# Kernel optimization log

Measured on AMD Instinct MI355X. Metric: run time of the kernel, lower is better.

Reference implementation:

```python
import jax, jax.numpy as jnp
import numpy as np

N_SPANS = 4096
EMB_DIM = 384
HEADS = 4
DECAY_LAMBDA = 5.0
THRESHOLD = 0.1
NEG_SLOPE = 0.2  # PyG GATConv default leaky_relu slope


def setup_inputs() -> dict:
    key = jax.random.key(0)
    k1, k2, k3, k4, k5, k6 = jax.random.split(key, 6)
    embeddings = jax.random.normal(k1, (N_SPANS, EMB_DIM), dtype=jnp.float32)
    span_positions = jnp.sort(
        jax.random.randint(k2, (N_SPANS, 2), 0, 100000), axis=1
    ).astype(jnp.int64)
    # GATConv params: lin (no bias), per-head attention vectors, output bias
    glorot = 1.0 / np.sqrt(EMB_DIM)
    W = jax.random.normal(k3, (EMB_DIM, HEADS, EMB_DIM), dtype=jnp.float32) * glorot
    att_src = jax.random.normal(k4, (HEADS, EMB_DIM), dtype=jnp.float32) * glorot
    att_dst = jax.random.normal(k5, (HEADS, EMB_DIM), dtype=jnp.float32) * glorot
    bias = jnp.zeros((EMB_DIM,), dtype=jnp.float32)
    return {
        "embeddings": embeddings,
        "span_positions": span_positions,
        "W": W,
        "att_src": att_src,
        "att_dst": att_dst,
        "bias": bias,
    }


def _adjacency_mask(embeddings):
    # A_ij = cos_sim(e_i, e_j) * exp(-|i - j| / lambda); edges where A > 0.1
    n = embeddings.shape[0]
    en = embeddings / jnp.linalg.norm(embeddings, axis=1, keepdims=True)
    cos_sim = en @ en.T  # [N, N]
    idx = jnp.arange(n, dtype=embeddings.dtype)
    decay = jnp.exp(-jnp.abs(idx[None, :] - idx[:, None]) / DECAY_LAMBDA)
    adj = cos_sim * decay
    # diagonal is 1.0 > threshold, so self-loops (required by GATConv) are present
    return adj > THRESHOLD  # symmetric mask: mask[i, j] == edge j -> i


def reference(embeddings, span_positions, W, att_src, att_dst, bias):
    mask = _adjacency_mask(embeddings)  # [N_dst, N_src]
    # GATConv(heads=4, concat=False): project, per-head additive attention
    x = jnp.einsum("nd,dhe->nhe", embeddings, W)  # [N, H, E]
    a_src = jnp.einsum("nhe,he->nh", x, att_src)  # [N, H]
    a_dst = jnp.einsum("nhe,he->nh", x, att_dst)  # [N, H]
    # logits[i, j, h] for edge j -> i
    logits = jax.nn.leaky_relu(a_dst[:, None, :] + a_src[None, :, :], NEG_SLOPE)
    logits = jnp.where(mask[:, :, None], logits, jnp.float32(-jnp.inf))
    alpha = jax.nn.softmax(logits, axis=1)  # softmax over incoming sources j
    out = jnp.einsum("ijh,jhe->ihe", alpha, x)  # [N, H, E]
    out = out.mean(axis=1) + bias  # concat=False -> mean over heads, then bias
    return out
```

## Files before the change

### kernel.cpp

```cpp
#include <hip/hip_runtime.h>
#include <hip/hip_bf16.h>
#include <math.h>

#define N_SPANS 4096
#define EMB 384
#define HEADS 4
#define HE (HEADS * EMB)
#define BAND 11
#define BW (2 * BAND + 1)

typedef short bf16x8 __attribute__((ext_vector_type(8)));
typedef float f32x4 __attribute__((ext_vector_type(4)));

__device__ __forceinline__ unsigned short f2bf(float f) {
    union { float f; unsigned u; } x; x.f = f;
    unsigned r = x.u + 0x7fffu + ((x.u >> 16) & 1u);
    return (unsigned short)(r >> 16);
}
__device__ __forceinline__ float bf2f(unsigned short u) {
    union { unsigned u; float f; } x; x.u = ((unsigned)u) << 16; return x.f;
}

__device__ __forceinline__ float wave_sum(float v) {
    #pragma unroll
    for (int off = 32; off; off >>= 1) v += __shfl_xor(v, off, 64);
    return v;
}
__device__ __forceinline__ float wave_max(float v) {
    #pragma unroll
    for (int off = 32; off; off >>= 1) v = fmaxf(v, __shfl_xor(v, off, 64));
    return v;
}

__device__ __forceinline__ void gl2lds16(const void* g, void* l) {
    __builtin_amdgcn_global_load_lds(
        (const __attribute__((address_space(1))) void*)(uintptr_t)g,
        (__attribute__((address_space(3))) void*)(unsigned)(uintptr_t)l,
        16, 0, 0);
}

__global__ __launch_bounds__(256) void prep(const float* __restrict__ E,
                                            const float* __restrict__ W,
                                            unsigned short* __restrict__ Ebf,
                                            unsigned short* __restrict__ Wt,
                                            float* __restrict__ invn,
                                            float* __restrict__ Dots,
                                            float* __restrict__ attacc) {
    __shared__ float tile[32][33];
    const int b = blockIdx.x;
    const int tid = threadIdx.x;
    if (b < 1024) {
        const int lane = tid & 63, w = tid >> 6;
        const int n = b * 4 + w;
        const float* er = E + (size_t)n * EMB;
        const int dmax = (n >= N_SPANS - BAND) ? (N_SPANS - 1 - n) : BAND;
        const float* nb[BAND];
        #pragma unroll
        for (int d = 1; d <= BAND; ++d) {
            int j = n + d; if (j > N_SPANS - 1) j = N_SPANS - 1;
            nb[d - 1] = E + (size_t)j * EMB;
        }
        float acc[12];
        #pragma unroll
        for (int d = 0; d < 12; ++d) acc[d] = 0.f;
        float ev[6];
        #pragma unroll
        for (int m = 0; m < 6; ++m) {
            const int k = m * 64 + lane;
            const float v = er[k];
            ev[m] = v;
            acc[0] += v * v;
            #pragma unroll
            for (int d = 1; d <= BAND; ++d) {
                float u = nb[d - 1][k];
                acc[d] += (d <= dmax) ? v * u : 0.f;
            }
        }
        #pragma unroll
        for (int m = 0; m < 6; ++m)
            Ebf[(size_t)n * EMB + m * 64 + lane] = f2bf(ev[m]);
        #pragma unroll
        for (int d = 0; d < 12; ++d) acc[d] = wave_sum(acc[d]);
        float dval = 0.f;
        #pragma unroll
        for (int d = 1; d <= BAND; ++d) if (lane == d) dval = acc[d];
        if (lane >= 1 && lane <= BAND) Dots[(size_t)n * 12 + lane] = dval;
        if (lane == 0) invn[n] = 1.0f / sqrtf(acc[0]);
    } else if (b < 1600) {
        const int t = b - 1024;
        const int n0 = (t % 48) * 32;
        const int k0 = (t / 48) * 32;
        const int tx = tid & 31, ty = tid >> 5;
        #pragma unroll
        for (int q = 0; q < 4; ++q)
            tile[ty + q * 8][tx] = W[(k0 + ty + q * 8) * HE + n0 + tx];
        __syncthreads();
        #pragma unroll
        for (int q = 0; q < 4; ++q)
            Wt[(n0 + ty + q * 8) * EMB + k0 + tx] = f2bf(tile[tx][ty + q * 8]);
    } else {
        const int t = b - 1600;
        ((float4*)attacc)[t * 256 + tid] = make_float4(0.f, 0.f, 0.f, 0.f);
    }
}

__global__ __launch_bounds__(256) void gemm_attn(const unsigned short* __restrict__ Ebf,
                                                 const unsigned short* __restrict__ Wt,
                                                 const float* __restrict__ attS,
                                                 const float* __restrict__ attD,
                                                 unsigned short* __restrict__ Xb,
                                                 float* __restrict__ asrc,
                                                 float* __restrict__ adst) {
    __shared__ unsigned short As[128 * 32];
    __shared__ unsigned short Bs[128 * 32];
    const int tid = threadIdx.x;
    const int lane = tid & 63;
    const int wave = tid >> 6;
    const int m0 = blockIdx.y * 128;
    const int n0 = blockIdx.x * 128;
    const int wr = (wave >> 1) * 64;
    const int wc = (wave & 1) * 64;
    const int quad = lane >> 4;
    const int l16 = lane & 15;

    const char* Ab = (const char*)Ebf + (size_t)(m0 + wave * 32 + (lane >> 2)) * 768 + (lane & 3) * 16;
    const char* Bb = (const char*)Wt  + (size_t)(n0 + wave * 32 + (lane >> 2)) * 768 + (lane & 3) * 16;
    char* AsB = (char*)As + wave * 32 * 64;
    char* BsB = (char*)Bs + wave * 32 * 64;

    f32x4 acc[4][4];
    #pragma unroll
    for (int i = 0; i < 4; ++i)
        #pragma unroll
        for (int j = 0; j < 4; ++j) acc[i][j] = 0.f;

    for (int kt = 0; kt < 12; ++kt) {
        const int kb = kt * 64;
        __syncthreads();
        gl2lds16(Ab + kb,            AsB);
        gl2lds16(Ab + kb + 16 * 768, AsB + 16 * 64);
        gl2lds16(Bb + kb,            BsB);
        gl2lds16(Bb + kb + 16 * 768, BsB + 16 * 64);
        __syncthreads();

        bf16x8 af[4], bfr[4];
        #pragma unroll
        for (int t = 0; t < 4; ++t) {
            af[t]  = *(const bf16x8*)(&As[(wr + t * 16 + l16) * 32 + quad * 8]);
            bfr[t] = *(const bf16x8*)(&Bs[(wc + t * 16 + l16) * 32 + quad * 8]);
        }
        #pragma unroll
        for (int ti = 0; ti < 4; ++ti)
            #pragma unroll
            for (int tj = 0; tj < 4; ++tj)
                acc[ti][tj] = __builtin_amdgcn_mfma_f32_16x16x32_bf16(
                    af[ti], bfr[tj], acc[ti][tj], 0, 0, 0);
    }

    const int hblk = (n0 + wc) / EMB;
    float aS[4], aD[4];
    #pragma unroll
    for (int tj = 0; tj < 4; ++tj) {
        int col = n0 + wc + tj * 16 + l16;
        aS[tj] = attS[col];
        aD[tj] = attD[col];
    }
    #pragma unroll
    for (int ti = 0; ti < 4; ++ti)
        #pragma unroll
        for (int r = 0; r < 4; ++r) {
            float ps = 0.f, pd = 0.f;
            #pragma unroll
            for (int tj = 0; tj < 4; ++tj) {
                float v = acc[ti][tj][r];
                ps += v * aS[tj];
                pd += v * aD[tj];
            }
            #pragma unroll
            for (int off = 1; off < 16; off <<= 1) {
                ps += __shfl_xor(ps, off, 64);
                pd += __shfl_xor(pd, off, 64);
            }
            if (l16 == 0) {
                int row = m0 + wr + ti * 16 + quad * 4 + r;
                atomicAdd(&asrc[row * HEADS + hblk], ps);
                atomicAdd(&adst[row * HEADS + hblk], pd);
            }
        }

    #pragma unroll
    for (int ti = 0; ti < 4; ++ti)
        #pragma unroll
        for (int tj = 0; tj < 4; ++tj) {
            int col = n0 + wc + tj * 16 + l16;
            #pragma unroll
            for (int r = 0; r < 4; ++r) {
                int row = m0 + wr + ti * 16 + quad * 4 + r;
                Xb[row * HE + col] = f2bf(acc[ti][tj][r]);
            }
        }
}

__global__ __launch_bounds__(256) void band_attn(const float* __restrict__ invn,
                                                 const float* __restrict__ Dots,
                                                 const float* __restrict__ asrc,
                                                 const float* __restrict__ adst,
                                                 const unsigned short* __restrict__ Xb,
                                                 const float* __restrict__ bias,
                                                 float* __restrict__ out) {
    __shared__ float sAl[4][BW][4];
    __shared__ int sList[4][24];
    const int tid = threadIdx.x, lane = tid & 63, w = tid >> 6;
    const int i = blockIdx.x * 4 + w;
    const int jo = lane;
    const int j = i - BAND + jo;
    const bool inb = (jo < BW) && (j >= 0) && (j < N_SPANS);
    const int jc = inb ? j : i;

    float dotv = 0.f;
    if (inb) {
        if (jo < BAND)      dotv = Dots[(size_t)j * 12 + (BAND - jo)];
        else if (jo > BAND) dotv = Dots[(size_t)i * 12 + (jo - BAND)];
    }
    bool flag;
    if (jo == BAND) {
        flag = true;
    } else {
        int dd = jo < BAND ? BAND - jo : jo - BAND;
        float a = ((dotv * invn[i]) * invn[jc]) * expf(-(float)dd * 0.2f);
        flag = inb && (a > 0.1f);
    }

    unsigned long long mbits = __ballot(flag);
    const int cnt = __popcll(mbits);
    const int rank = __popcll(mbits & ((1ull << jo) - 1ull));
    if (flag) sList[w][rank] = jo;

    const float4 ad = ((const float4*)adst)[i];
    const float4 as = inb ? ((const float4*)asrc)[jc] : make_float4(0.f, 0.f, 0.f, 0.f);
    float al[4];
    #pragma unroll
    for (int h = 0; h < 4; ++h) {
        float z = (&ad.x)[h] + (&as.x)[h];
        z = (z >= 0.f) ? z : 0.2f * z;
        float lg = flag ? z : -INFINITY;
        float mx = wave_max(lg);
        float ex = flag ? expf(lg - mx) : 0.f;
        float sm = wave_sum(ex);
        al[h] = ex / sm;
    }
    if (flag) *(float4*)&sAl[w][jo][0] = make_float4(al[0], al[1], al[2], al[3]);

    #pragma unroll
    for (int m = 0; m < 6; ++m) {
        const int e = m * 64 + lane;
        float acc = 0.f;
        for (int ii = 0; ii < cnt; ++ii) {
            const int joL = sList[w][ii];
            const int jj = i - BAND + joL;
            const float4 a4 = *(const float4*)&sAl[w][joL][0];
            const unsigned short* xr = Xb + (size_t)jj * HE + e;
            acc += a4.x * bf2f(xr[0])   + a4.y * bf2f(xr[384])
                 + a4.z * bf2f(xr[768]) + a4.w * bf2f(xr[1152]);
        }
        out[i * EMB + e] = 0.25f * acc + bias[e];
    }
}

extern "C" void kernel_launch(void* const* d_in, const int* in_sizes, int n_in,
                              void* d_out, int out_size, void* d_ws, size_t ws_size,
                              hipStream_t stream) {
    const float* E       = (const float*)d_in[0];
    const float* W       = (const float*)d_in[2];
    const float* att_src = (const float*)d_in[3];
    const float* att_dst = (const float*)d_in[4];
    const float* bias    = (const float*)d_in[5];
    float* out = (float*)d_out;

    char* ws = (char*)d_ws;
    unsigned short* Xb  = (unsigned short*)ws;
    unsigned short* Ebf = (unsigned short*)(ws + 12582912);
    unsigned short* Wt  = (unsigned short*)(ws + 15728640);
    float* invn         = (float*)(ws + 16908288);
    float* asrc         = (float*)(ws + 16924672);
    float* adst         = (float*)(ws + 16990208);
    float* Dots         = (float*)(ws + 17055744);

    prep<<<1632, 256, 0, stream>>>(E, W, Ebf, Wt, invn, Dots, asrc );
    gemm_attn<<<dim3(12, 32), 256, 0, stream>>>(Ebf, Wt, att_src, att_dst, Xb, asrc, adst);
    band_attn<<<1024, 256, 0, stream>>>(invn, Dots, asrc, adst, Xb, bias, out);
}
```

Before: 108.7 us.

## Double-buffer LDS tiles in projection GEMM with wider K steps

New measurement: 113.5 us. +4.4%, slower.

```diff
diff --git a/kernel.cpp b/kernel.cpp
--- a/kernel.cpp
+++ b/kernel.cpp
@@ -111,22 +111,30 @@
                                                  unsigned short* __restrict__ Xb,
                                                  float* __restrict__ asrc,
                                                  float* __restrict__ adst) {
-    __shared__ unsigned short As[128 * 32];
-    __shared__ unsigned short Bs[128 * 32];
+    __shared__ unsigned short As[2][8192];
+    __shared__ unsigned short Bs[2][8192];
     const int tid = threadIdx.x;
     const int lane = tid & 63;
     const int wave = tid >> 6;
+    const int quad = lane >> 4;
+    const int l16 = lane & 15;
     const int m0 = blockIdx.y * 128;
     const int n0 = blockIdx.x * 128;
     const int wr = (wave >> 1) * 64;
     const int wc = (wave & 1) * 64;
-    const int quad = lane >> 4;
-    const int l16 = lane & 15;
-
-    const char* Ab = (const char*)Ebf + (size_t)(m0 + wave * 32 + (lane >> 2)) * 768 + (lane & 3) * 16;
-    const char* Bb = (const char*)Wt  + (size_t)(n0 + wave * 32 + (lane >> 2)) * 768 + (lane & 3) * 16;
-    char* AsB = (char*)As + wave * 32 * 64;
-    char* BsB = (char*)Bs + wave * 32 * 64;
+    const int wrB = (wave >> 1) * 8192;
+    const int wcB = (wave & 1) * 8192;
+
+    const char* aSrc[4];
+    const char* bSrc[4];
+    #pragma unroll
+    for (int q = 0; q < 4; ++q) {
+        const int c = wave * 4 + q;
+        const int rg = c >> 1;
+        const int klo = (c & 1) * 4 + quad;
+        aSrc[q] = (const char*)Ebf + (size_t)(m0 + rg * 16 + l16) * 768 + klo * 16;
+        bSrc[q] = (const char*)Wt  + (size_t)(n0 + rg * 16 + l16) * 768 + klo * 16;
+    }
 
     f32x4 acc[4][4];
     #pragma unroll
@@ -134,27 +142,47 @@
         #pragma unroll
         for (int j = 0; j < 4; ++j) acc[i][j] = 0.f;
 
-    for (int kt = 0; kt < 12; ++kt) {
-        const int kb = kt * 64;
+    #pragma unroll
+    for (int q = 0; q < 4; ++q) {
+        const int c = wave * 4 + q;
+        gl2lds16(aSrc[q], (char*)As[0] + c * 1024);
+        gl2lds16(bSrc[q], (char*)Bs[0] + c * 1024);
+    }
+    __syncthreads();
+
+    int cur = 0;
+    for (int kt = 0; kt < 6; ++kt) {
+        if (kt < 5) {
+            const int kb = (kt + 1) * 128;
+            #pragma unroll
+            for (int q = 0; q < 4; ++q) {
+                const int c = wave * 4 + q;
+                gl2lds16(aSrc[q] + kb, (char*)As[cur ^ 1] + c * 1024);
+                gl2lds16(bSrc[q] + kb, (char*)Bs[cur ^ 1] + c * 1024);
+            }
+        }
+
+        const char* aR = (const char*)As[cur] + wrB + lane * 16;
+        const char* bR = (const char*)Bs[cur] + wcB + lane * 16;
+        bf16x8 af[2][4], bfr[2][4];
+        #pragma unroll
+        for (int kk = 0; kk < 2; ++kk)
+            #pragma unroll
+            for (int t = 0; t < 4; ++t) {
+                af[kk][t]  = *(const bf16x8*)(aR + t * 2048 + kk * 1024);
+                bfr[kk][t] = *(const bf16x8*)(bR + t * 2048 + kk * 1024);
+            }
+        #pragma unroll
+        for (int kk = 0; kk < 2; ++kk)
+            #pragma unroll
+            for (int ti = 0; ti < 4; ++ti)
+                #pragma unroll
+                for (int tj = 0; tj < 4; ++tj)
+                    acc[ti][tj] = __builtin_amdgcn_mfma_f32_16x16x32_bf16(
+                        af[kk][ti], bfr[kk][tj], acc[ti][tj], 0, 0, 0);
+
         __syncthreads();
-        gl2lds16(Ab + kb,            AsB);
-        gl2lds16(Ab + kb + 16 * 768, AsB + 16 * 64);
-        gl2lds16(Bb + kb,            BsB);
-        gl2lds16(Bb + kb + 16 * 768, BsB + 16 * 64);
-        __syncthreads();
-
-        bf16x8 af[4], bfr[4];
-        #pragma unroll
-        for (int t = 0; t < 4; ++t) {
-            af[t]  = *(const bf16x8*)(&As[(wr + t * 16 + l16) * 32 + quad * 8]);
-            bfr[t] = *(const bf16x8*)(&Bs[(wc + t * 16 + l16) * 32 + quad * 8]);
-        }
-        #pragma unroll
-        for (int ti = 0; ti < 4; ++ti)
-            #pragma unroll
-            for (int tj = 0; tj < 4; ++tj)
-                acc[ti][tj] = __builtin_amdgcn_mfma_f32_16x16x32_bf16(
-                    af[ti], bfr[tj], acc[ti][tj], 0, 0, 0);
+        cur ^= 1;
     }
 
     const int hblk = (n0 + wc) / EMB;
```

## Fuse prep, GEMM and band attention into one cooperative persistent kernel

Applied to the files above, without the earlier changes.

New measurement: 230.1 us. 112% more time.

```diff
diff --git a/kernel.cpp b/kernel.cpp
--- a/kernel.cpp
+++ b/kernel.cpp
@@ -1,6 +1,9 @@
 #include <hip/hip_runtime.h>
+#include <hip/hip_cooperative_groups.h>
 #include <hip/hip_bf16.h>
 #include <math.h>
+
+namespace cg = cooperative_groups;
 
 #define N_SPANS 4096
 #define EMB 384
@@ -37,6 +40,240 @@
         (const __attribute__((address_space(1))) void*)(uintptr_t)g,
         (__attribute__((address_space(3))) void*)(unsigned)(uintptr_t)l,
         16, 0, 0);
+}
+
+__global__ __launch_bounds__(256, 2) void fused(
+    const float* __restrict__ E, const float* __restrict__ W,
+    const float* __restrict__ attS, const float* __restrict__ attD,
+    const float* __restrict__ bias,
+    unsigned short* __restrict__ Ebf, unsigned short* __restrict__ Wt,
+    float* __restrict__ invn, float* __restrict__ Dots,
+    unsigned short* __restrict__ Xb, float* __restrict__ asrc,
+    float* __restrict__ adst, float* __restrict__ out)
+{
+    __shared__ union {
+        float tile[32][33];
+        struct { unsigned short As[128 * 32]; unsigned short Bs[128 * 32]; } g;
+        struct { float sAl[4][BW][4]; int sList[4][24]; } c;
+    } sh;
+
+    cg::grid_group grid = cg::this_grid();
+    const int tid = threadIdx.x, lane = tid & 63, w = tid >> 6;
+    const int b = blockIdx.x;
+
+    for (int n = b * 4 + w; n < N_SPANS; n += 1536) {
+        const float4* er4 = (const float4*)(E + (size_t)n * EMB);
+        const int dmax = (n >= N_SPANS - BAND) ? (N_SPANS - 1 - n) : BAND;
+        const float4* nb4[BAND];
+        #pragma unroll
+        for (int d = 1; d <= BAND; ++d) {
+            int j = n + d; if (j > N_SPANS - 1) j = N_SPANS - 1;
+            nb4[d - 1] = (const float4*)(E + (size_t)j * EMB);
+        }
+        float acc[12];
+        #pragma unroll
+        for (int d = 0; d < 12; ++d) acc[d] = 0.f;
+        #pragma unroll
+        for (int mq = 0; mq < 2; ++mq) {
+            const int idx = mq * 64 + lane;
+            if (idx < 96) {
+                float4 v = er4[idx];
+                acc[0] += v.x * v.x + v.y * v.y + v.z * v.z + v.w * v.w;
+                ushort4 pb;
+                pb.x = f2bf(v.x); pb.y = f2bf(v.y); pb.z = f2bf(v.z); pb.w = f2bf(v.w);
+                ((ushort4*)(Ebf + (size_t)n * EMB))[idx] = pb;
+                #pragma unroll
+                for (int d = 1; d <= BAND; ++d) {
+                    float4 u = nb4[d - 1][idx];
+                    float dd = v.x * u.x + v.y * u.y + v.z * u.z + v.w * u.w;
+                    acc[d] += (d <= dmax) ? dd : 0.f;
+                }
+            }
+        }
+        #pragma unroll
+        for (int d = 0; d < 12; ++d) acc[d] = wave_sum(acc[d]);
+        float dval = 0.f;
+        #pragma unroll
+        for (int d = 1; d <= BAND; ++d) if (lane == d) dval = acc[d];
+        if (lane >= 1 && lane <= BAND) Dots[(size_t)n * 12 + lane] = dval;
+        if (lane == 0) invn[n] = 1.0f / sqrtf(acc[0]);
+    }
+
+    {
+        const int tx = tid & 31, ty = tid >> 5;
+        for (int t = b; t < 576; t += 384) {
+            const int n0t = (t % 48) * 32, k0 = (t / 48) * 32;
+            __syncthreads();
+            #pragma unroll
+            for (int q = 0; q < 4; ++q)
+                sh.tile[ty + q * 8][tx] = W[(k0 + ty + q * 8) * HE + n0t + tx];
+            __syncthreads();
+            #pragma unroll
+            for (int q = 0; q < 4; ++q)
+                Wt[(n0t + ty + q * 8) * EMB + k0 + tx] = f2bf(sh.tile[tx][ty + q * 8]);
+        }
+    }
+
+    if (b >= 192 && b < 224)
+        ((float4*)asrc)[(b - 192) * 256 + tid] = make_float4(0.f, 0.f, 0.f, 0.f);
+
+    grid.sync();
+
+    {
+        const int m0 = (b / 12) * 128;
+        const int n0 = (b % 12) * 128;
+        const int wave = w;
+        const int quad = lane >> 4;
+        const int l16 = lane & 15;
+        const int wr = (wave >> 1) * 64;
+        const int wc = (wave & 1) * 64;
+
+        const char* Ab = (const char*)Ebf + (size_t)(m0 + wave * 32 + (lane >> 2)) * 768 + (lane & 3) * 16;
+        const char* Bb = (const char*)Wt  + (size_t)(n0 + wave * 32 + (lane >> 2)) * 768 + (lane & 3) * 16;
+        char* AsB = (char*)sh.g.As + wave * 32 * 64;
+        char* BsB = (char*)sh.g.Bs + wave * 32 * 64;
+
+        f32x4 acc[4][4];
+        #pragma unroll
+        for (int i = 0; i < 4; ++i)
+            #pragma unroll
+            for (int j = 0; j < 4; ++j) acc[i][j] = 0.f;
+
+        for (int kt = 0; kt < 12; ++kt) {
+            const int kb = kt * 64;
+            __syncthreads();
+            gl2lds16(Ab + kb,            AsB);
+            gl2lds16(Ab + kb + 16 * 768, AsB + 16 * 64);
+            gl2lds16(Bb + kb,            BsB);
+            gl2lds16(Bb + kb + 16 * 768, BsB + 16 * 64);
+            __syncthreads();
+
+            bf16x8 af[4], bfr[4];
+            #pragma unroll
+            for (int t = 0; t < 4; ++t) {
+                af[t]  = *(const bf16x8*)(&sh.g.As[(wr + t * 16 + l16) * 32 + quad * 8]);
+                bfr[t] = *(const bf16x8*)(&sh.g.Bs[(wc + t * 16 + l16) * 32 + quad * 8]);
+            }
+            #pragma unroll
+            for (int ti = 0; ti < 4; ++ti)
+                #pragma unroll
+                for (int tj = 0; tj < 4; ++tj)
+                    acc[ti][tj] = __builtin_amdgcn_mfma_f32_16x16x32_bf16(
+                        af[ti], bfr[tj], acc[ti][tj], 0, 0, 0);
+        }
+
+        const int hblk = (n0 + wc) / EMB;
+        float aS[4], aD[4];
+        #pragma unroll
+        for (int tj = 0; tj < 4; ++tj) {
+            int col = n0 + wc + tj * 16 + l16;
+            aS[tj] = attS[col];
+            aD[tj] = attD[col];
+        }
+        #pragma unroll
+        for (int ti = 0; ti < 4; ++ti)
+            #pragma unroll
+            for (int r = 0; r < 4; ++r) {
+                float ps = 0.f, pd = 0.f;
+                #pragma unroll
+                for (int tj = 0; tj < 4; ++tj) {
+                    float v = acc[ti][tj][r];
+                    ps += v * aS[tj];
+                    pd += v * aD[tj];
+                }
+                #pragma unroll
+                for (int off = 1; off < 16; off <<= 1) {
+                    ps += __shfl_xor(ps, off, 64);
+                    pd += __shfl_xor(pd, off, 64);
+                }
+                if (l16 == 0) {
+                    int row = m0 + wr + ti * 16 + quad * 4 + r;
+                    atomicAdd(&asrc[row * HEADS + hblk], ps);
+                    atomicAdd(&adst[row * HEADS + hblk], pd);
+                }
+            }
+
+        #pragma unroll
+        for (int ti = 0; ti < 4; ++ti)
+            #pragma unroll
+            for (int tj = 0; tj < 4; ++tj) {
+                int col = n0 + wc + tj * 16 + l16;
+                #pragma unroll
+                for (int r = 0; r < 4; ++r) {
+                    int row = m0 + wr + ti * 16 + quad * 4 + r;
+                    Xb[row * HE + col] = f2bf(acc[ti][tj][r]);
+                }
+            }
+    }
+
+    grid.sync();
+
+    for (int i = b * 4 + w; i < N_SPANS; i += 1536) {
+        const int jo = lane;
+        const int j = i - BAND + jo;
+        const bool inb = (jo < BW) && (j >= 0) && (j < N_SPANS);
+        const int jc = inb ? j : i;
+
+        float dotv = 0.f;
+        if (inb) {
+            if (jo < BAND)      dotv = Dots[(size_t)j * 12 + (BAND - jo)];
+            else if (jo > BAND) dotv = Dots[(size_t)i * 12 + (jo - BAND)];
+        }
+        bool flag;
+        if (jo == BAND) {
+            flag = true;
+        } else {
+            int dd = jo < BAND ? BAND - jo : jo - BAND;
+            float a = ((dotv * invn[i]) * invn[jc]) * expf(-(float)dd * 0.2f);
+            flag = inb && (a > 0.1f);
+        }
+
+        unsigned long long mbits = __ballot(flag);
+        const int cnt = __popcll(mbits);
+        const int rank = __popcll(mbits & ((1ull << jo) - 1ull));
+        if (flag) sh.c.sList[w][rank] = jo;
+
+        const float4 ad = ((const float4*)adst)[i];
+        const float4 as = inb ? ((const float4*)asrc)[jc] : make_float4(0.f, 0.f, 0.f, 0.f);
+        float al[4];
+        #pragma unroll
+        for (int h = 0; h < 4; ++h) {
+            float z = (&ad.x)[h] + (&as.x)[h];
+            z = (z >= 0.f) ? z : 0.2f * z;
+            float lg = flag ? z : -INFINITY;
+            float mx = wave_max(lg);
+            float ex = flag ? expf(lg - mx) : 0.f;
+            float sm = wave_sum(ex);
+            al[h] = ex / sm;
+        }
+        if (flag) *(float4*)&sh.c.sAl[w][jo][0] = make_float4(al[0], al[1], al[2], al[3]);
+
+        #pragma unroll
+        for (int mq = 0; mq < 2; ++mq) {
+            const int e4 = mq * 64 + lane;
+            if (e4 < 96) {
+                float4 a = make_float4(0.f, 0.f, 0.f, 0.f);
+                for (int ii = 0; ii < cnt; ++ii) {
+                    const int joL = sh.c.sList[w][ii];
+                    const int jj = i - BAND + joL;
+                    const float4 a4 = *(const float4*)&sh.c.sAl[w][joL][0];
+                    const ushort4* xr = (const ushort4*)(Xb + (size_t)jj * HE);
+                    ushort4 h0 = xr[e4], h1 = xr[e4 + 96], h2 = xr[e4 + 192], h3 = xr[e4 + 288];
+                    a.x += a4.x * bf2f(h0.x) + a4.y * bf2f(h1.x) + a4.z * bf2f(h2.x) + a4.w * bf2f(h3.x);
+                    a.y += a4.x * bf2f(h0.y) + a4.y * bf2f(h1.y) + a4.z * bf2f(h2.y) + a4.w * bf2f(h3.y);
+                    a.z += a4.x * bf2f(h0.z) + a4.y * bf2f(h1.z) + a4.z * bf2f(h2.z) + a4.w * bf2f(h3.z);
+                    a.w += a4.x * bf2f(h0.w) + a4.y * bf2f(h1.w) + a4.z * bf2f(h2.w) + a4.w * bf2f(h3.w);
+                }
+                const float4 bv = ((const float4*)bias)[e4];
+                float4 o;
+                o.x = 0.25f * a.x + bv.x;
+                o.y = 0.25f * a.y + bv.y;
+                o.z = 0.25f * a.z + bv.z;
+                o.w = 0.25f * a.w + bv.w;
+                ((float4*)(out + (size_t)i * EMB))[e4] = o;
+            }
+        }
+    }
 }
 
 __global__ __launch_bounds__(256) void prep(const float* __restrict__ E,
@@ -286,7 +523,14 @@
     float* adst         = (float*)(ws + 16990208);
     float* Dots         = (float*)(ws + 17055744);
 
-    prep<<<1632, 256, 0, stream>>>(E, W, Ebf, Wt, invn, Dots, asrc );
-    gemm_attn<<<dim3(12, 32), 256, 0, stream>>>(Ebf, Wt, att_src, att_dst, Xb, asrc, adst);
-    band_attn<<<1024, 256, 0, stream>>>(invn, Dots, asrc, adst, Xb, bias, out);
-}
+    void* args[] = {(void*)&E, (void*)&W, (void*)&att_src, (void*)&att_dst,
+                    (void*)&bias, (void*)&Ebf, (void*)&Wt, (void*)&invn,
+                    (void*)&Dots, (void*)&Xb, (void*)&asrc, (void*)&adst, (void*)&out};
+    hipError_t err = hipLaunchCooperativeKernel((const void*)fused, dim3(384), dim3(256),
+                                                args, 0, stream);
+    if (err != hipSuccess) {
+        prep<<<1632, 256, 0, stream>>>(E, W, Ebf, Wt, invn, Dots, asrc);
+        gemm_attn<<<dim3(12, 32), 256, 0, stream>>>(Ebf, Wt, att_src, att_dst, Xb, asrc, adst);
+        band_attn<<<1024, 256, 0, stream>>>(invn, Dots, asrc, adst, Xb, bias, out);
+    }
+}
```
